# Kernel tuning notes

Hardware: AMD Instinct MI355X
Metric: run time of the kernel (lower is better)

Reference implementation:

```python
import jax, jax.numpy as jnp
import numpy as np

BS, PV, NPTS, C = 8, 40000, 32, 4   # batch, pillars/sample (=max_voxels), max_num_points, point channels
X_L, Y_L = 432, 496                  # BEV grid from voxel_size / point_cloud_range


def setup_inputs() -> dict:
    key = jax.random.key(0)
    k1, k2, k3 = jax.random.split(key, 3)
    # (P, num_points, c) voxelized point features
    pillars = jax.random.normal(k1, (BS * PV, NPTS, C), dtype=jnp.float32)
    # unique BEV cell per pillar within each sample (voxelizer never emits duplicate coords)
    perms = jax.vmap(lambda k: jax.random.permutation(k, X_L * Y_L)[:PV])(
        jax.random.split(k2, BS))  # (BS, PV) linear cell ids
    xs = (perms // Y_L).reshape(-1)
    ys = (perms % Y_L).reshape(-1)
    b = jnp.repeat(jnp.arange(BS, dtype=jnp.int32), PV)
    z = jnp.zeros_like(b)
    coors_batch = jnp.stack([b, xs.astype(jnp.int32), ys.astype(jnp.int32), z], axis=1)  # (P, 4)
    npoints_per_pillar = jax.random.randint(k3, (BS * PV,), 1, NPTS + 1, dtype=jnp.int32)
    return {
        "pillars": pillars,
        "coors_batch": coors_batch,
        "npoints_per_pillar": npoints_per_pillar,
        "bs": BS, "x_l": X_L, "y_l": Y_L,
    }


def reference(pillars, coors_batch, npoints_per_pillar, bs, x_l, y_l):
    # per-pillar xyz center of mass: sum over (zero-padded) points / true point count
    center_pt = jnp.sum(pillars[:, :, :3], axis=1) / npoints_per_pillar[:, None].astype(jnp.float32)  # (P, 3)
    # scatter centers into dense BEV canvas (bs, x_l, y_l, 3); coords unique -> set semantics match torch assignment
    canvas = jnp.zeros((bs, x_l, y_l, 3), dtype=jnp.float32)
    canvas = canvas.at[coors_batch[:, 0], coors_batch[:, 1], coors_batch[:, 2]].set(center_pt)
    # per-sample permute(2,1,0): (x_l,y_l,3) -> (3,y_l,x_l)
    batched_pillar_center = jnp.transpose(canvas, (0, 3, 2, 1))
    return (pillars, coors_batch, npoints_per_pillar, batched_pillar_center)
```

## Files before the change

kernel.cpp:

```cpp
#include <hip/hip_runtime.h>


__global__ __launch_bounds__(256) void canvas_zero(float4* __restrict__ dst, long n4) {
    long i = (long)blockIdx.x * blockDim.x + threadIdx.x;
    const long stride = (long)gridDim.x * blockDim.x;
    const float4 z = make_float4(0.f, 0.f, 0.f, 0.f);
    for (; i < n4; i += stride) dst[i] = z;
}

__global__ __launch_bounds__(256) void pillar_fused(
    const float4* __restrict__ pillars4,
    const int4* __restrict__ coors4,
    const int* __restrict__ npoints,
    const int* __restrict__ xlp,
    const int* __restrict__ ylp,
    float4* __restrict__ out_pillars4,
    float4* __restrict__ out_coors4,
    float* __restrict__ out_np,
    float* __restrict__ canvas,
    int P)
{
    const int group = blockIdx.x * (blockDim.x >> 5) + (threadIdx.x >> 5);
    const int lane  = threadIdx.x & 31;
    if (group >= P) return;
    const int p = group;

    const float4 v = pillars4[p * 32 + lane];
    out_pillars4[p * 32 + lane] = v;

    float sx = v.x, sy = v.y, sz = v.z;
    #pragma unroll
    for (int m = 16; m >= 1; m >>= 1) {
        sx += __shfl_xor(sx, m);
        sy += __shfl_xor(sy, m);
        sz += __shfl_xor(sz, m);
    }

    if (lane == 0) {
        const int4 c = coors4[p];
        out_coors4[p] = make_float4((float)c.x, (float)c.y, (float)c.z, (float)c.w);

        const int npts = npoints[p];
        out_np[p] = (float)npts;
        const float inv = 1.0f / (float)npts;

        const int x_l = *xlp;
        const int y_l = *ylp;

        const long cs   = (long)y_l * (long)x_l;
        const long base = (long)c.x * 3l * cs + (long)c.z * (long)x_l + (long)c.y;
        canvas[base]          = sx * inv;
        canvas[base + cs]     = sy * inv;
        canvas[base + 2 * cs] = sz * inv;
    }
}

extern "C" void kernel_launch(void* const* d_in, const int* in_sizes, int n_in,
                              void* d_out, int out_size, void* d_ws, size_t ws_size,
                              hipStream_t stream) {
    const float4* pillars4 = (const float4*)d_in[0];
    const int4* coors4     = (const int4*)d_in[1];
    const int* npoints     = (const int*)d_in[2];
    const int* xlp = (const int*)d_in[4];
    const int* ylp = (const int*)d_in[5];

    const int n_pillars = in_sizes[0];
    const int n_coors   = in_sizes[1];
    const int P         = in_sizes[2];

    float* out            = (float*)d_out;
    float4* out_pillars4  = (float4*)out;
    float* out_coors      = out + n_pillars;
    float* out_np         = out_coors + n_coors;
    float* canvas         = out_np + P;
    const long canvas_elems = (long)out_size - (long)n_pillars - (long)n_coors - (long)P;

    const long n4 = canvas_elems >> 2;
    const int zblocks = (int)((n4 + 255) / 256);
    canvas_zero<<<zblocks, 256, 0, stream>>>((float4*)canvas, n4);

    const int groups_per_block = 256 / 32;
    const int blocks = (P + groups_per_block - 1) / groups_per_block;
    pillar_fused<<<blocks, 256, 0, stream>>>(
        pillars4, coors4, npoints, xlp, ylp,
        out_pillars4, (float4*)out_coors, out_np, canvas, P);
}
```

Before: 79.54 us.

## Replace canvas zero-fill and scatter with index map plus coalesced gather

Instead of zeroing the dense canvas and scattering three strided writes per pillar, pillars write their centers and a cell-to-pillar index map in workspace. A gather kernel then writes each canvas cell exactly once with vectorized coalesced stores. This avoids the full zero pass and the uncoalesced scatter, but adds an index-map zero pass, an extra kernel launch and random center reads. It falls back to the old path if the workspace is too small.

```diff
diff --git a/kernel.cpp b/kernel.cpp
--- a/kernel.cpp
+++ b/kernel.cpp
@@ -1,11 +1,9 @@
 #include <hip/hip_runtime.h>
 
 
-__global__ __launch_bounds__(256) void canvas_zero(float4* __restrict__ dst, long n4) {
-    long i = (long)blockIdx.x * blockDim.x + threadIdx.x;
-    const long stride = (long)gridDim.x * blockDim.x;
-    const float4 z = make_float4(0.f, 0.f, 0.f, 0.f);
-    for (; i < n4; i += stride) dst[i] = z;
+__global__ __launch_bounds__(256) void idx_zero(int4* __restrict__ dst, int n4) {
+    int i = blockIdx.x * 256 + threadIdx.x;
+    if (i < n4) dst[i] = make_int4(0, 0, 0, 0);
 }
 
 __global__ __launch_bounds__(256) void pillar_fused(
@@ -17,7 +15,8 @@
     float4* __restrict__ out_pillars4,
     float4* __restrict__ out_coors4,
     float* __restrict__ out_np,
-    float* __restrict__ canvas,
+    float4* __restrict__ centers,
+    int* __restrict__ idx,
     int P)
 {
     const int group = blockIdx.x * (blockDim.x >> 5) + (threadIdx.x >> 5);
@@ -44,14 +43,80 @@
         out_np[p] = (float)npts;
         const float inv = 1.0f / (float)npts;
 
+        centers[p] = make_float4(sx * inv, sy * inv, sz * inv, 0.f);
+
         const int x_l = *xlp;
         const int y_l = *ylp;
+        idx[c.x * (y_l * x_l) + c.z * x_l + c.y] = p + 1;
+    }
+}
 
-        const long cs   = (long)y_l * (long)x_l;
-        const long base = (long)c.x * 3l * cs + (long)c.z * (long)x_l + (long)c.y;
-        canvas[base]          = sx * inv;
-        canvas[base + cs]     = sy * inv;
-        canvas[base + 2 * cs] = sz * inv;
+__global__ __launch_bounds__(256) void canvas_gather(
+    const int4* __restrict__ idx4,
+    const float4* __restrict__ centers,
+    float4* __restrict__ canvas4,
+    const int* __restrict__ xlp,
+    const int* __restrict__ ylp,
+    int ncells4)
+{
+    int i = blockIdx.x * 256 + threadIdx.x;
+    if (i >= ncells4) return;
+
+    const int cs4 = (*xlp * *ylp) >> 2;
+    const int b   = i / cs4;
+    const int r4  = i - b * cs4;
+
+    const int4 id = idx4[i];
+    float4 wx = make_float4(0.f, 0.f, 0.f, 0.f);
+    float4 wy = wx, wz = wx;
+    if (id.x > 0) { float4 c = centers[id.x - 1]; wx.x = c.x; wy.x = c.y; wz.x = c.z; }
+    if (id.y > 0) { float4 c = centers[id.y - 1]; wx.y = c.x; wy.y = c.y; wz.y = c.z; }
+    if (id.z > 0) { float4 c = centers[id.z - 1]; wx.z = c.x; wy.z = c.y; wz.z = c.z; }
+    if (id.w > 0) { float4 c = centers[id.w - 1]; wx.w = c.x; wy.w = c.y; wz.w = c.z; }
+
+    const long base = (long)(b * 3) * cs4 + r4;
+    canvas4[base]           = wx;
+    canvas4[base + cs4]     = wy;
+    canvas4[base + 2 * cs4] = wz;
+}
+
+__global__ __launch_bounds__(256) void canvas_zero(float4* __restrict__ dst, long n4) {
+    long i = (long)blockIdx.x * blockDim.x + threadIdx.x;
+    const long stride = (long)gridDim.x * blockDim.x;
+    const float4 z = make_float4(0.f, 0.f, 0.f, 0.f);
+    for (; i < n4; i += stride) dst[i] = z;
+}
+
+__global__ __launch_bounds__(256) void pillar_fused_scatter(
+    const float4* __restrict__ pillars4, const int4* __restrict__ coors4,
+    const int* __restrict__ npoints, const int* __restrict__ xlp,
+    const int* __restrict__ ylp, float4* __restrict__ out_pillars4,
+    float4* __restrict__ out_coors4, float* __restrict__ out_np,
+    float* __restrict__ canvas, int P)
+{
+    const int group = blockIdx.x * (blockDim.x >> 5) + (threadIdx.x >> 5);
+    const int lane  = threadIdx.x & 31;
+    if (group >= P) return;
+    const int p = group;
+    const float4 v = pillars4[p * 32 + lane];
+    out_pillars4[p * 32 + lane] = v;
+    float sx = v.x, sy = v.y, sz = v.z;
+    #pragma unroll
+    for (int m = 16; m >= 1; m >>= 1) {
+        sx += __shfl_xor(sx, m);
+        sy += __shfl_xor(sy, m);
+        sz += __shfl_xor(sz, m);
+    }
+    if (lane == 0) {
+        const int4 c = coors4[p];
+        out_coors4[p] = make_float4((float)c.x, (float)c.y, (float)c.z, (float)c.w);
+        const int npts = npoints[p];
+        out_np[p] = (float)npts;
+        const float inv = 1.0f / (float)npts;
+        const int x_l = *xlp, y_l = *ylp;
+        const long cs = (long)y_l * x_l;
+        const long base = (long)c.x * 3l * cs + (long)c.z * x_l + (long)c.y;
+        canvas[base] = sx * inv; canvas[base + cs] = sy * inv; canvas[base + 2*cs] = sz * inv;
     }
 }
 
@@ -68,20 +133,34 @@
     const int n_coors   = in_sizes[1];
     const int P         = in_sizes[2];
 
-    float* out            = (float*)d_out;
-    float4* out_pillars4  = (float4*)out;
-    float* out_coors      = out + n_pillars;
-    float* out_np         = out_coors + n_coors;
-    float* canvas         = out_np + P;
-    const long canvas_elems = (long)out_size - (long)n_pillars - (long)n_coors - (long)P;
+    float* out           = (float*)d_out;
+    float4* out_pillars4 = (float4*)out;
+    float* out_coors     = out + n_pillars;
+    float* out_np        = out_coors + n_coors;
+    float* canvas        = out_np + P;
+    const long canvas_elems = (long)out_size - n_pillars - n_coors - P;
+    const long ncells       = canvas_elems / 3;
 
-    const long n4 = canvas_elems >> 2;
-    const int zblocks = (int)((n4 + 255) / 256);
-    canvas_zero<<<zblocks, 256, 0, stream>>>((float4*)canvas, n4);
-
+    const size_t ws_need = (size_t)P * 16 + (size_t)ncells * 4;
     const int groups_per_block = 256 / 32;
     const int blocks = (P + groups_per_block - 1) / groups_per_block;
-    pillar_fused<<<blocks, 256, 0, stream>>>(
-        pillars4, coors4, npoints, xlp, ylp,
-        out_pillars4, (float4*)out_coors, out_np, canvas, P);
+
+    if (ws_size >= ws_need && (ncells & 3) == 0) {
+        float4* centers = (float4*)d_ws;
+        int*    idx     = (int*)((char*)d_ws + (size_t)P * 16);
+        const int ncells4 = (int)(ncells >> 2);
+
+        idx_zero<<<(ncells4 + 255) / 256, 256, 0, stream>>>((int4*)idx, ncells4);
+        pillar_fused<<<blocks, 256, 0, stream>>>(
+            pillars4, coors4, npoints, xlp, ylp,
+            out_pillars4, (float4*)out_coors, out_np, centers, idx, P);
+        canvas_gather<<<(ncells4 + 255) / 256, 256, 0, stream>>>(
+            (const int4*)idx, centers, (float4*)canvas, xlp, ylp, ncells4);
+    } else {
+        const long n4 = canvas_elems >> 2;
+        canvas_zero<<<(int)((n4 + 255) / 256), 256, 0, stream>>>((float4*)canvas, n4);
+        pillar_fused_scatter<<<blocks, 256, 0, stream>>>(
+            pillars4, coors4, npoints, xlp, ylp,
+            out_pillars4, (float4*)out_coors, out_np, canvas, P);
+    }
 }
```

Result: slower. 84.53 us (+6.3%).
